# Optimization experiments

Measured on AMD Instinct MI355X. Metric: run time of the kernel, lower is better.

## Reference

```python
import jax, jax.numpy as jnp
import numpy as np

B, T, C, H = 8, 1024, 1024, 16
D = C // H  # head_dim = 64


def setup_inputs() -> dict:
    key = jax.random.key(0)
    k1, k2, k3 = jax.random.split(key, 3)
    x = jax.random.normal(k1, (B, T, C), dtype=jnp.float32)
    # boolean causal mask: True = attend (PyTorch SDPA bool-mask semantics)
    attn_mask = jnp.tril(jnp.ones((T, T), dtype=jnp.bool_))[None, None, :, :]
    w_attn = jax.random.normal(k2, (C, 3 * C), dtype=jnp.float32) * (1.0 / np.sqrt(C))
    b_attn = jnp.zeros((3 * C,), dtype=jnp.float32)
    w_proj = jax.random.normal(k3, (C, C), dtype=jnp.float32) * (1.0 / np.sqrt(C))
    b_proj = jnp.zeros((C,), dtype=jnp.float32)
    return {"x": x, "attn_mask": attn_mask, "w_attn": w_attn, "b_attn": b_attn,
            "w_proj": w_proj, "b_proj": b_proj}


def reference(x, attn_mask, w_attn, b_attn, w_proj, b_proj):
    Bx, Tx, Cx = x.shape
    qkv = x @ w_attn + b_attn                      # [B,T,3C]
    q, k, v = jnp.split(qkv, 3, axis=-1)
    # [B,T,C] -> [B,H,T,D]
    q = q.reshape(Bx, Tx, H, D).transpose(0, 2, 1, 3)
    k = k.reshape(Bx, Tx, H, D).transpose(0, 2, 1, 3)
    v = v.reshape(Bx, Tx, H, D).transpose(0, 2, 1, 3)
    scale = 1.0 / jnp.sqrt(jnp.asarray(D, dtype=x.dtype))
    scores = jnp.einsum('bhqd,bhkd->bhqk', q, k) * scale  # [B,H,T,T]
    neg = jnp.asarray(jnp.finfo(x.dtype).min, dtype=x.dtype)
    scores = jnp.where(attn_mask, scores, neg)
    probs = jax.nn.softmax(scores, axis=-1)
    y = jnp.einsum('bhqk,bhkd->bhqd', probs, v)    # [B,H,T,D]
    y = y.transpose(0, 2, 1, 3).reshape(Bx, Tx, Cx)
    return y @ w_proj + b_proj
```

## Files before the change

### kernel.cpp

```cpp
#include <hip/hip_runtime.h>


typedef __bf16 bf16x8 __attribute__((ext_vector_type(8)));
typedef float f32x4 __attribute__((ext_vector_type(4)));
typedef unsigned uint4e __attribute__((ext_vector_type(4)));
typedef unsigned short ushort8e __attribute__((ext_vector_type(8)));

typedef __attribute__((address_space(1))) const unsigned as1_u32;
typedef __attribute__((address_space(3))) unsigned as3_u32;

#define NEG_INF (-__builtin_inff())

__device__ __forceinline__ unsigned short f2bf(float f) {
  unsigned u = __builtin_bit_cast(unsigned, f);
  u += 0x7fffu + ((u >> 16) & 1u);
  return (unsigned short)(u >> 16);
}


__global__ void cvt_x_kernel(const float* __restrict__ in, unsigned short* __restrict__ out) {
  size_t i = (size_t)(blockIdx.x * 256 + threadIdx.x) * 8;
  float4 a = *(const float4*)(in + i);
  float4 b = *(const float4*)(in + i + 4);
  ushort8e o;
  o[0] = f2bf(a.x); o[1] = f2bf(a.y); o[2] = f2bf(a.z); o[3] = f2bf(a.w);
  o[4] = f2bf(b.x); o[5] = f2bf(b.y); o[6] = f2bf(b.z); o[7] = f2bf(b.w);
  *(ushort8e*)(out + i) = o;
}

__global__ void cvt_wT_kernel(const float* __restrict__ w, unsigned short* __restrict__ wT,
                              int K, int N) {
  __shared__ float tile[32][33];
  const int n0 = blockIdx.x * 32, k0 = blockIdx.y * 32;
  const int tx = threadIdx.x, ty = threadIdx.y;
#pragma unroll
  for (int i = 0; i < 32; i += 8)
    tile[ty + i][tx] = w[(size_t)(k0 + ty + i) * N + n0 + tx];
  __syncthreads();
#pragma unroll
  for (int i = 0; i < 32; i += 8)
    wT[(size_t)(n0 + ty + i) * K + k0 + tx] = f2bf(tile[tx][ty + i]);
}


template <int EPI, int NTN>
__global__ __launch_bounds__(512, 2) void gemm_kernel(
    const unsigned short* __restrict__ A, const unsigned short* __restrict__ BT,
    const float* __restrict__ bias, float* __restrict__ outF,
    unsigned short* __restrict__ qO, unsigned short* __restrict__ kO,
    unsigned short* __restrict__ vO, int M, int N, int K) {
  constexpr int NT = 16;
  __shared__ __align__(16) unsigned short LDS[2][32768];

  const int tid = threadIdx.x;
  const int w = tid >> 6, lane = tid & 63;
  const int g = lane >> 4, cx = lane & 15;

  constexpr int CPX = NTN * 32 / 8;
  const int bid = blockIdx.x;
  const int wg = (bid & 7) * CPX + (bid >> 3);
  const int bm = (wg / NTN) * 256, bn = (wg % NTN) * 256;

  const int wm = (w >> 2) * 128;
  const int wn = (w & 3) * 64;

  const int srow = tid >> 3;
  const int schunk = ((tid & 7) ^ (srow & 7)) << 3;
  const unsigned short* gA = A + (size_t)(bm + srow) * K + schunk;
  const unsigned short* gB = BT + (size_t)(bn + srow) * K + schunk;
  const int ldst = w * 8 * 64;

  auto issueA = [&](int i, int t) {
    __builtin_amdgcn_global_load_lds(
        (as1_u32*)(const void*)(gA + (size_t)i * 64 * K + t * 64),
        (as3_u32*)(void*)&LDS[t & 1][i * 4096 + ldst], 16, 0, 0);
  };
  auto issueB = [&](int i, int t) {
    __builtin_amdgcn_global_load_lds(
        (as1_u32*)(const void*)(gB + (size_t)i * 64 * K + t * 64),
        (as3_u32*)(void*)&LDS[t & 1][16384 + i * 4096 + ldst], 16, 0, 0);
  };

  f32x4 acc[8][4] = {};
  const int rsw = cx & 7;

  issueB(0, 0); issueB(1, 0); issueB(2, 0); issueB(3, 0);
  issueA(0, 0); issueA(2, 0); issueA(1, 0); issueA(3, 0);

  for (int t = 0; t < NT; ++t) {
    const unsigned short* Lb = &LDS[t & 1][0];
    asm volatile("s_waitcnt vmcnt(2)" ::: "memory");
    __builtin_amdgcn_s_barrier();
    asm volatile("" ::: "memory");
    if (t + 1 < NT) { issueB(0, t + 1); issueB(1, t + 1); }
    bf16x8 bfr[4][2];
#pragma unroll
    for (int nf = 0; nf < 4; ++nf) {
      const int RB = wn + nf * 16 + cx;
#pragma unroll
      for (int ks = 0; ks < 2; ++ks)
        bfr[nf][ks] = *(const bf16x8*)&Lb[16384 + RB * 64 + (((ks * 4 + g) ^ rsw) << 3)];
    }
    {
      bf16x8 af[4][2];
#pragma unroll
      for (int mf = 0; mf < 4; ++mf) {
        const int R = wm + mf * 16 + cx;
#pragma unroll
        for (int ks = 0; ks < 2; ++ks)
          af[mf][ks] = *(const bf16x8*)&Lb[R * 64 + (((ks * 4 + g) ^ rsw) << 3)];
      }
      __builtin_amdgcn_s_setprio(1);
#pragma unroll
      for (int mf = 0; mf < 4; ++mf)
#pragma unroll
        for (int nf = 0; nf < 2; ++nf)
#pragma unroll
          for (int ks = 0; ks < 2; ++ks)
            acc[mf][nf] = __builtin_amdgcn_mfma_f32_16x16x32_bf16(
                af[mf][ks], bfr[nf][ks], acc[mf][nf], 0, 0, 0);
      __builtin_amdgcn_s_setprio(0);
      if (t + 1 < NT) { issueB(2, t + 1); issueB(3, t + 1); }
      __builtin_amdgcn_s_setprio(1);
#pragma unroll
      for (int mf = 0; mf < 4; ++mf)
#pragma unroll
        for (int nf = 2; nf < 4; ++nf)
#pragma unroll
          for (int ks = 0; ks < 2; ++ks)
            acc[mf][nf] = __builtin_amdgcn_mfma_f32_16x16x32_bf16(
                af[mf][ks], bfr[nf][ks], acc[mf][nf], 0, 0, 0);
      __builtin_amdgcn_s_setprio(0);
    }
    if (t + 1 < NT) asm volatile("s_waitcnt vmcnt(4)" ::: "memory");
    else            asm volatile("s_waitcnt vmcnt(0)" ::: "memory");
    __builtin_amdgcn_s_barrier();
    asm volatile("" ::: "memory");
    if (t + 1 < NT) { issueA(0, t + 1); issueA(2, t + 1); }
    {
      bf16x8 af[4][2];
#pragma unroll
      for (int mf = 0; mf < 4; ++mf) {
        const int R = wm + 64 + mf * 16 + cx;
#pragma unroll
        for (int ks = 0; ks < 2; ++ks)
          af[mf][ks] = *(const bf16x8*)&Lb[R * 64 + (((ks * 4 + g) ^ rsw) << 3)];
      }
      __builtin_amdgcn_s_setprio(1);
#pragma unroll
      for (int mf = 0; mf < 4; ++mf)
#pragma unroll
        for (int nf = 0; nf < 2; ++nf)
#pragma unroll
          for (int ks = 0; ks < 2; ++ks)
            acc[mf + 4][nf] = __builtin_amdgcn_mfma_f32_16x16x32_bf16(
                af[mf][ks], bfr[nf][ks], acc[mf + 4][nf], 0, 0, 0);
      __builtin_amdgcn_s_setprio(0);
      if (t + 1 < NT) { issueA(1, t + 1); issueA(3, t + 1); }
      __builtin_amdgcn_s_setprio(1);
#pragma unroll
      for (int mf = 0; mf < 4; ++mf)
#pragma unroll
        for (int nf = 2; nf < 4; ++nf)
#pragma unroll
          for (int ks = 0; ks < 2; ++ks)
            acc[mf + 4][nf] = __builtin_amdgcn_mfma_f32_16x16x32_bf16(
                af[mf][ks], bfr[nf][ks], acc[mf + 4][nf], 0, 0, 0);
      __builtin_amdgcn_s_setprio(0);
    }
  }

  if (EPI == 0) {
#pragma unroll
    for (int mf = 0; mf < 8; ++mf) {
      const int m0 = bm + wm + mf * 16 + (g << 2);
      const int b = m0 >> 10, t0 = m0 & 1023;
#pragma unroll
      for (int nf = 0; nf < 4; ++nf) {
        const int n = bn + wn + nf * 16 + cx;
        const float bv = bias[n];
        const int which = n >> 10, rem = n & 1023;
        const int h = rem >> 6, d = rem & 63;
        const int bh = b * 16 + h;
        f32x4& a4 = acc[mf][nf];
        if (which == 2) {
          uint2 pv;
          pv.x = (unsigned)f2bf(a4[0] + bv) | ((unsigned)f2bf(a4[1] + bv) << 16);
          pv.y = (unsigned)f2bf(a4[2] + bv) | ((unsigned)f2bf(a4[3] + bv) << 16);
          *(uint2*)(vO + ((size_t)bh * 64 + d) * 1024 + t0) = pv;
        } else {
          unsigned short* dst = (which == 0 ? qO : kO);
          const float scl = (which == 0) ? 0.18033688011112042f : 1.0f;
#pragma unroll
          for (int r = 0; r < 4; ++r)
            dst[((size_t)bh * 1024 + (t0 + r)) * 64 + d] = f2bf((a4[r] + bv) * scl);
        }
      }
    }
  } else {
#pragma unroll
    for (int mf = 0; mf < 8; ++mf) {
      const int m0 = bm + wm + mf * 16 + (g << 2);
#pragma unroll
      for (int nf = 0; nf < 4; ++nf) {
        const int n = bn + wn + nf * 16 + cx;
        const float bv = bias[n];
        f32x4& a4 = acc[mf][nf];
#pragma unroll
        for (int r = 0; r < 4; ++r)
          outF[(size_t)(m0 + r) * N + n] = a4[r] + bv;
      }
    }
  }
}


__global__ __launch_bounds__(256) void attn_kernel(
    const unsigned short* __restrict__ qB, const unsigned short* __restrict__ kB,
    const unsigned short* __restrict__ vB, unsigned short* __restrict__ yB) {
  __shared__ __align__(16) unsigned short Ks[2][64 * 64];
  __shared__ __align__(16) unsigned short Vs[2][64 * 64];
  const int lane = threadIdx.x & 63, w = threadIdx.x >> 6;
  const int g = lane >> 4, cx = lane & 15;
  const int bh = blockIdx.x;
  const int qt = 7 - blockIdx.y;
  const int qb0 = qt * 128;
  const int nt = qt * 2 + 2;
  const unsigned short* Qh = qB + (size_t)bh * 65536;
  const unsigned short* Kh = kB + (size_t)bh * 65536;
  const unsigned short* Vh = vB + (size_t)bh * 65536;

  const int qsb0 = qb0 + w * 16, qsb1 = qb0 + 64 + w * 16;

  bf16x8 qf[2][2];
#pragma unroll
  for (int s = 0; s < 2; ++s) {
    const int qq = (s ? qsb1 : qsb0) + cx;
#pragma unroll
    for (int h = 0; h < 2; ++h)
      qf[s][h] = *(const bf16x8*)(Qh + (size_t)qq * 64 + h * 32 + g * 8);
  }

  f32x4 oacc[2][4] = {};
  float mrun0 = NEG_INF, mrun1 = NEG_INF, L0 = 0.f, L1 = 0.f;

  const int srl = lane >> 3, sch = lane & 7;

  auto stage = [&](int t, int buf) {
#pragma unroll
    for (int i = 0; i < 2; ++i) {
      const int row = w * 16 + i * 8 + srl;
      const int csw = (sch ^ (row & 7)) << 3;
      const unsigned short* gk = Kh + (size_t)(t * 64 + row) * 64 + csw;
      __builtin_amdgcn_global_load_lds((as1_u32*)(const void*)gk,
          (as3_u32*)(void*)&Ks[buf][(w * 16 + i * 8) * 64], 16, 0, 0);
      const unsigned short* gv = Vh + (size_t)row * 1024 + t * 64 + csw;
      __builtin_amdgcn_global_load_lds((as1_u32*)(const void*)gv,
          (as3_u32*)(void*)&Vs[buf][(w * 16 + i * 8) * 64], 16, 0, 0);
    }
  };

  auto mkpf = [&](const float* pp) -> bf16x8 {
    unsigned lo0 = (unsigned)f2bf(pp[0]) | ((unsigned)f2bf(pp[1]) << 16);
    unsigned hi0 = (unsigned)f2bf(pp[2]) | ((unsigned)f2bf(pp[3]) << 16);
    unsigned lo1 = (unsigned)f2bf(pp[4]) | ((unsigned)f2bf(pp[5]) << 16);
    unsigned hi1 = (unsigned)f2bf(pp[6]) | ((unsigned)f2bf(pp[7]) << 16);
    const int s0 = ((g & 1) << 5) + cx, s1 = s0 + 16;
    unsigned a0 = __shfl(lo0, s0), a1 = __shfl(hi0, s0), a2 = __shfl(lo0, s1), a3 = __shfl(hi0, s1);
    unsigned b0 = __shfl(lo1, s0), b1 = __shfl(hi1, s0), b2 = __shfl(lo1, s1), b3 = __shfl(hi1, s1);
    const bool chh = g >= 2;
    uint4e pw;
    pw[0] = chh ? b0 : a0; pw[1] = chh ? b1 : a1; pw[2] = chh ? b2 : a2; pw[3] = chh ? b3 : a3;
    return __builtin_bit_cast(bf16x8, pw);
  };

  stage(0, 0);
  asm volatile("s_waitcnt vmcnt(0)" ::: "memory");
  __builtin_amdgcn_s_barrier();
  asm volatile("" ::: "memory");

  for (int t = 0; t < nt; ++t) {
    const int buf = t & 1;
    if (t + 1 < nt) stage(t + 1, buf ^ 1);
    const int k0 = t * 64;
    const bool act0 = k0 <= qsb0 + 15;

    bf16x8 kf[4][2];
#pragma unroll
    for (int kc = 0; kc < 4; ++kc) {
      const int row = kc * 16 + cx;
#pragma unroll
      for (int h = 0; h < 2; ++h)
        kf[kc][h] = *(const bf16x8*)&Ks[buf][row * 64 + (((h * 4 + g) ^ (row & 7)) << 3)];
    }
    f32x4 sa[2][4];
#pragma unroll
    for (int kc = 0; kc < 4; ++kc) {
      f32x4 z = {0.f, 0.f, 0.f, 0.f};
      sa[1][kc] = __builtin_amdgcn_mfma_f32_16x16x32_bf16(kf[kc][0], qf[1][0], z, 0, 0, 0);
      sa[1][kc] = __builtin_amdgcn_mfma_f32_16x16x32_bf16(kf[kc][1], qf[1][1], sa[1][kc], 0, 0, 0);
    }
    if (act0) {
#pragma unroll
      for (int kc = 0; kc < 4; ++kc) {
        f32x4 z = {0.f, 0.f, 0.f, 0.f};
        sa[0][kc] = __builtin_amdgcn_mfma_f32_16x16x32_bf16(kf[kc][0], qf[0][0], z, 0, 0, 0);
        sa[0][kc] = __builtin_amdgcn_mfma_f32_16x16x32_bf16(kf[kc][1], qf[0][1], sa[0][kc], 0, 0, 0);
      }
    }

    bf16x8 vf[4][2];
#pragma unroll
    for (int db = 0; db < 4; ++db) {
      const int row = db * 16 + cx;
#pragma unroll
      for (int h = 0; h < 2; ++h)
        vf[db][h] = *(const bf16x8*)&Vs[buf][row * 64 + (((h * 4 + g) ^ (row & 7)) << 3)];
    }

#pragma unroll
    for (int s = 0; s < 2; ++s) {
      if (s == 0 && !act0) continue;
      const int qsb = s ? qsb1 : qsb0;
      const int qg = qsb + cx;
      float& mrun = s ? mrun1 : mrun0;
      float& L = s ? L1 : L0;
      float p[16];
      const bool straddle = (k0 + 63) > qsb;
#pragma unroll
      for (int kc = 0; kc < 4; ++kc)
#pragma unroll
        for (int r = 0; r < 4; ++r) {
          float v = sa[s][kc][r];
          if (straddle && (k0 + kc * 16 + (g << 2) + r) > qg) v = NEG_INF;
          p[kc * 4 + r] = v;
        }
      float m01 = fmaxf(fmaxf(p[0], p[1]), fmaxf(p[2], p[3]));
      float m23 = fmaxf(fmaxf(p[4], p[5]), fmaxf(p[6], p[7]));
      float m45 = fmaxf(fmaxf(p[8], p[9]), fmaxf(p[10], p[11]));
      float m67 = fmaxf(fmaxf(p[12], p[13]), fmaxf(p[14], p[15]));
      float pm = fmaxf(fmaxf(m01, m23), fmaxf(m45, m67));
      pm = fmaxf(pm, __shfl_xor(pm, 16));
      pm = fmaxf(pm, __shfl_xor(pm, 32));
      const float mnew = fmaxf(mrun, pm);
      const float cs = __builtin_amdgcn_exp2f(mrun - mnew);
      mrun = mnew;
      float ps = 0.f;
#pragma unroll
      for (int e = 0; e < 16; ++e) {
        p[e] = __builtin_amdgcn_exp2f(p[e] - mnew);
        ps += p[e];
      }
      ps += __shfl_xor(ps, 16);
      ps += __shfl_xor(ps, 32);
      L = L * cs + ps;
#pragma unroll
      for (int db = 0; db < 4; ++db) {
        oacc[s][db][0] *= cs; oacc[s][db][1] *= cs;
        oacc[s][db][2] *= cs; oacc[s][db][3] *= cs;
      }
      const bf16x8 pf0 = mkpf(p);
      const bf16x8 pf1 = mkpf(p + 8);
#pragma unroll
      for (int db = 0; db < 4; ++db) {
        oacc[s][db] = __builtin_amdgcn_mfma_f32_16x16x32_bf16(vf[db][0], pf0, oacc[s][db], 0, 0, 0);
        oacc[s][db] = __builtin_amdgcn_mfma_f32_16x16x32_bf16(vf[db][1], pf1, oacc[s][db], 0, 0, 0);
      }
    }

    asm volatile("s_waitcnt vmcnt(0)" ::: "memory");
    __builtin_amdgcn_s_barrier();
    asm volatile("" ::: "memory");
  }

  const int b = bh >> 4, h = bh & 15;
#pragma unroll
  for (int s = 0; s < 2; ++s) {
    const float inv = 1.0f / (s ? L1 : L0);
    const int qg = (s ? qsb1 : qsb0) + cx;
    unsigned short* yp = yB + (size_t)(b * 1024 + qg) * 1024 + h * 64;
#pragma unroll
    for (int db = 0; db < 4; ++db) {
      uint2 pv;
      pv.x = (unsigned)f2bf(oacc[s][db][0] * inv) | ((unsigned)f2bf(oacc[s][db][1] * inv) << 16);
      pv.y = (unsigned)f2bf(oacc[s][db][2] * inv) | ((unsigned)f2bf(oacc[s][db][3] * inv) << 16);
      *(uint2*)(yp + db * 16 + (g << 2)) = pv;
    }
  }
}


extern "C" void kernel_launch(void* const* d_in, const int* in_sizes, int n_in,
                              void* d_out, int out_size, void* d_ws, size_t ws_size,
                              hipStream_t stream) {
  (void)in_sizes; (void)n_in; (void)out_size; (void)ws_size;
  const float* x = (const float*)d_in[0];
  const float* w_attn = (const float*)d_in[2];
  const float* b_attn = (const float*)d_in[3];
  const float* w_proj = (const float*)d_in[4];
  const float* b_proj = (const float*)d_in[5];
  float* out = (float*)d_out;

  char* ws = (char*)d_ws;
  unsigned short* xb     = (unsigned short*)(ws);
  unsigned short* wqkvT  = (unsigned short*)(ws + 16777216);
  unsigned short* wprojT = (unsigned short*)(ws + 23068672);
  unsigned short* qb     = (unsigned short*)(ws + 25165824);
  unsigned short* kb     = (unsigned short*)(ws + 41943040);
  unsigned short* vtb    = (unsigned short*)(ws + 58720256);
  unsigned short* yb     = (unsigned short*)(ws + 75497472);

  cvt_x_kernel<<<4096, 256, 0, stream>>>(x, xb);
  cvt_wT_kernel<<<dim3(96, 32), dim3(32, 8), 0, stream>>>(w_attn, wqkvT, 1024, 3072);
  cvt_wT_kernel<<<dim3(32, 32), dim3(32, 8), 0, stream>>>(w_proj, wprojT, 1024, 1024);

  gemm_kernel<0, 12><<<384, 512, 0, stream>>>(xb, wqkvT, b_attn, nullptr,
                                              qb, kb, vtb, 8192, 3072, 1024);
  attn_kernel<<<dim3(128, 8), 256, 0, stream>>>(qb, kb, vtb, yb);
  gemm_kernel<1, 4><<<128, 512, 0, stream>>>(yb, wprojT, b_proj, out,
                                             nullptr, nullptr, nullptr, 8192, 1024, 1024);
}
```

Baseline: 165.9 us.

## Restructure GEMM main loop into two-tile unrolled pipeline with deeper prefetch

Rewrites the bf16 MFMA GEMM main loop to process two K-tiles per iteration, with both LDS buffers preloaded up front. Loads for tile t+2 are issued into a buffer once its fragments have been read. The compute is split into four quadrant MFMA groups separated by workgroup barriers, and the A and B fragment reads are interleaved with the global-to-LDS issues. The aim is to hide more global load latency by keeping loads further ahead. The cost is more barriers per tile and fragment arrays hoisted outside the loop, which may raise synchronisation overhead and register pressure.

```diff
diff --git a/kernel.cpp b/kernel.cpp
--- a/kernel.cpp
+++ b/kernel.cpp
@@ -68,7 +68,7 @@
   const int schunk = ((tid & 7) ^ (srow & 7)) << 3;
   const unsigned short* gA = A + (size_t)(bm + srow) * K + schunk;
   const unsigned short* gB = BT + (size_t)(bn + srow) * K + schunk;
-  const int ldst = w * 8 * 64;
+  const int ldst = w * 512;
 
   auto issueA = [&](int i, int t) {
     __builtin_amdgcn_global_load_lds(
@@ -82,92 +82,90 @@
   };
 
   f32x4 acc[8][4] = {};
+  bf16x8 af[4][2], bfr[4][2];
   const int rsw = cx & 7;
 
-  issueB(0, 0); issueB(1, 0); issueB(2, 0); issueB(3, 0);
-  issueA(0, 0); issueA(2, 0); issueA(1, 0); issueA(3, 0);
-
-  for (int t = 0; t < NT; ++t) {
-    const unsigned short* Lb = &LDS[t & 1][0];
-    asm volatile("s_waitcnt vmcnt(2)" ::: "memory");
+  auto bar = [&] {
+    asm volatile("" ::: "memory");
     __builtin_amdgcn_s_barrier();
     asm volatile("" ::: "memory");
-    if (t + 1 < NT) { issueB(0, t + 1); issueB(1, t + 1); }
-    bf16x8 bfr[4][2];
-#pragma unroll
-    for (int nf = 0; nf < 4; ++nf) {
-      const int RB = wn + nf * 16 + cx;
+  };
+  auto rdA = [&](const unsigned short* Lb, int mbase) {
+#pragma unroll
+    for (int mf = 0; mf < 4; ++mf) {
+      const int R = wm + mbase + mf * 16 + cx;
 #pragma unroll
       for (int ks = 0; ks < 2; ++ks)
-        bfr[nf][ks] = *(const bf16x8*)&Lb[16384 + RB * 64 + (((ks * 4 + g) ^ rsw) << 3)];
-    }
-    {
-      bf16x8 af[4][2];
-#pragma unroll
-      for (int mf = 0; mf < 4; ++mf) {
-        const int R = wm + mf * 16 + cx;
+        af[mf][ks] = *(const bf16x8*)&Lb[R * 64 + (((ks * 4 + g) ^ rsw) << 3)];
+    }
+  };
+  auto rdB = [&](const unsigned short* Lb, int nfb) {
+#pragma unroll
+    for (int nf = 0; nf < 2; ++nf) {
+      const int RB = wn + (nfb + nf) * 16 + cx;
+#pragma unroll
+      for (int ks = 0; ks < 2; ++ks)
+        bfr[nfb + nf][ks] =
+            *(const bf16x8*)&Lb[16384 + RB * 64 + (((ks * 4 + g) ^ rsw) << 3)];
+    }
+  };
+  auto quad = [&](int ar, int nb) {
+    __builtin_amdgcn_s_setprio(1);
+#pragma unroll
+    for (int mf = 0; mf < 4; ++mf)
+#pragma unroll
+      for (int nf = 0; nf < 2; ++nf)
 #pragma unroll
         for (int ks = 0; ks < 2; ++ks)
-          af[mf][ks] = *(const bf16x8*)&Lb[R * 64 + (((ks * 4 + g) ^ rsw) << 3)];
-      }
-      __builtin_amdgcn_s_setprio(1);
-#pragma unroll
-      for (int mf = 0; mf < 4; ++mf)
-#pragma unroll
-        for (int nf = 0; nf < 2; ++nf)
-#pragma unroll
-          for (int ks = 0; ks < 2; ++ks)
-            acc[mf][nf] = __builtin_amdgcn_mfma_f32_16x16x32_bf16(
-                af[mf][ks], bfr[nf][ks], acc[mf][nf], 0, 0, 0);
-      __builtin_amdgcn_s_setprio(0);
-      if (t + 1 < NT) { issueB(2, t + 1); issueB(3, t + 1); }
-      __builtin_amdgcn_s_setprio(1);
-#pragma unroll
-      for (int mf = 0; mf < 4; ++mf)
-#pragma unroll
-        for (int nf = 2; nf < 4; ++nf)
-#pragma unroll
-          for (int ks = 0; ks < 2; ++ks)
-            acc[mf][nf] = __builtin_amdgcn_mfma_f32_16x16x32_bf16(
-                af[mf][ks], bfr[nf][ks], acc[mf][nf], 0, 0, 0);
-      __builtin_amdgcn_s_setprio(0);
-    }
-    if (t + 1 < NT) asm volatile("s_waitcnt vmcnt(4)" ::: "memory");
-    else            asm volatile("s_waitcnt vmcnt(0)" ::: "memory");
-    __builtin_amdgcn_s_barrier();
-    asm volatile("" ::: "memory");
-    if (t + 1 < NT) { issueA(0, t + 1); issueA(2, t + 1); }
-    {
-      bf16x8 af[4][2];
-#pragma unroll
-      for (int mf = 0; mf < 4; ++mf) {
-        const int R = wm + 64 + mf * 16 + cx;
-#pragma unroll
-        for (int ks = 0; ks < 2; ++ks)
-          af[mf][ks] = *(const bf16x8*)&Lb[R * 64 + (((ks * 4 + g) ^ rsw) << 3)];
-      }
-      __builtin_amdgcn_s_setprio(1);
-#pragma unroll
-      for (int mf = 0; mf < 4; ++mf)
-#pragma unroll
-        for (int nf = 0; nf < 2; ++nf)
-#pragma unroll
-          for (int ks = 0; ks < 2; ++ks)
-            acc[mf + 4][nf] = __builtin_amdgcn_mfma_f32_16x16x32_bf16(
-                af[mf][ks], bfr[nf][ks], acc[mf + 4][nf], 0, 0, 0);
-      __builtin_amdgcn_s_setprio(0);
-      if (t + 1 < NT) { issueA(1, t + 1); issueA(3, t + 1); }
-      __builtin_amdgcn_s_setprio(1);
-#pragma unroll
-      for (int mf = 0; mf < 4; ++mf)
-#pragma unroll
-        for (int nf = 2; nf < 4; ++nf)
-#pragma unroll
-          for (int ks = 0; ks < 2; ++ks)
-            acc[mf + 4][nf] = __builtin_amdgcn_mfma_f32_16x16x32_bf16(
-                af[mf][ks], bfr[nf][ks], acc[mf + 4][nf], 0, 0, 0);
-      __builtin_amdgcn_s_setprio(0);
-    }
+          acc[ar + mf][nb + nf] = __builtin_amdgcn_mfma_f32_16x16x32_bf16(
+              af[mf][ks], bfr[nb + nf][ks], acc[ar + mf][nb + nf], 0, 0, 0);
+    __builtin_amdgcn_s_setprio(0);
+  };
+
+  issueB(0, 0); issueB(1, 0); issueB(2, 0); issueB(3, 0);
+  issueA(0, 0); issueA(1, 0); issueA(2, 0); issueA(3, 0);
+  issueB(0, 1); issueB(1, 1); issueB(2, 1); issueB(3, 1);
+  issueA(0, 1); issueA(1, 1); issueA(2, 1); issueA(3, 1);
+
+  for (int it = 0; it < NT / 2; ++it) {
+    const int t0 = 2 * it, t1 = t0 + 1;
+    const bool stg = (it < NT / 2 - 1);
+    const unsigned short* L0 = &LDS[0][0];
+    const unsigned short* L1 = &LDS[1][0];
+
+    asm volatile("s_waitcnt vmcnt(8)" ::: "memory");
+    bar();
+    rdA(L0, 0); rdB(L0, 0);
+    quad(0, 0);
+    bar();
+    rdB(L0, 2);
+    quad(0, 2);
+    bar();
+    rdA(L0, 64);
+    if (stg) { issueB(0, t0 + 2); issueB(1, t0 + 2); }
+    quad(4, 0);
+    bar();
+    if (stg) { issueB(2, t0 + 2); issueB(3, t0 + 2); }
+    quad(4, 2);
+    bar();
+    if (stg) asm volatile("s_waitcnt vmcnt(4)" ::: "memory");
+    else     asm volatile("s_waitcnt vmcnt(0)" ::: "memory");
+    bar();
+    rdA(L1, 0); rdB(L1, 0);
+    if (stg) { issueA(0, t0 + 2); issueA(1, t0 + 2); }
+    quad(0, 0);
+    bar();
+    rdB(L1, 2);
+    if (stg) { issueA(2, t0 + 2); issueA(3, t0 + 2); }
+    quad(0, 2);
+    bar();
+    rdA(L1, 64);
+    if (stg) { issueB(0, t1 + 2); issueB(1, t1 + 2); issueB(2, t1 + 2); issueB(3, t1 + 2); }
+    quad(4, 0);
+    bar();
+    if (stg) { issueA(0, t1 + 2); issueA(1, t1 + 2); issueA(2, t1 + 2); issueA(3, t1 + 2); }
+    quad(4, 2);
+    bar();
   }
 
   if (EPI == 0) {
```

After: 170.2 us. +2.6%, slower.
